# Performance work log

Hardware: AMD Instinct MI355X
Metric: run time of the kernel (lower is better)

## Reference

```python
import jax, jax.numpy as jnp
import numpy as np

KNN = 10       # knn_size
TOPK = 4       # top_k_select
H = 4          # num_heads
HID = 64       # edge-MLP hidden dim


def setup_inputs() -> dict:
    key = jax.random.key(0)
    ks = jax.random.split(key, 12)
    B, V, D = 4, 4096, 256
    s = 0.02
    return {
        "voxel_tokens": jax.random.normal(ks[0], (B, V, D), jnp.float32),
        "voxel_coords": jax.random.uniform(ks[1], (B, V, 3), jnp.float32) * 10.0,
        "mask": jnp.ones((B, V), dtype=bool),
        # EdgeScoringMLP: Linear(2D+3 -> 64), Linear(64 -> 1)
        "W1": jax.random.normal(ks[2], (2 * D + 3, HID), jnp.float32) * s,
        "b1": jnp.zeros((HID,), jnp.float32),
        "W2": jax.random.normal(ks[3], (HID, 1), jnp.float32) * s,
        "b2": jnp.zeros((1,), jnp.float32),
        # CrossAttention projections (D -> D)
        "Wq": jax.random.normal(ks[4], (D, D), jnp.float32) * s,
        "bq": jnp.zeros((D,), jnp.float32),
        "Wk": jax.random.normal(ks[5], (D, D), jnp.float32) * s,
        "bk": jnp.zeros((D,), jnp.float32),
        "Wv": jax.random.normal(ks[6], (D, D), jnp.float32) * s,
        "bv": jnp.zeros((D,), jnp.float32),
        "Wo": jax.random.normal(ks[7], (D, D), jnp.float32) * s,
        "bo": jnp.zeros((D,), jnp.float32),
    }


def reference(voxel_tokens, voxel_coords, mask,
              W1, b1, W2, b2, Wq, bq, Wk, bk, Wv, bv, Wo, bo):
    # mask is all-True (Vp == V per batch element), so the original per-batch
    # loop over dynamic voxel counts is an exact vmap over B. Dropouts are in
    # eval mode (identity).
    D = voxel_tokens.shape[-1]
    Dh = D // H

    def single(tok, coo):  # tok: (V, D), coo: (V, 3)
        # --- KNN graph build (squared euclidean; monotonic in true cdist) ---
        sq = jnp.sum(coo * coo, axis=-1)                        # (V,)
        d2 = sq[:, None] + sq[None, :] - 2.0 * (coo @ coo.T)    # (V, V)
        _, knn = jax.lax.top_k(-d2, KNN + 1)                    # smallest dists
        knn = knn[:, 1:]                                        # drop self, (V, KNN)

        # --- edge features: [anchor_tok, neighbor_tok, rel_pos] ---
        nb_tok = tok[knn]                                       # (V, KNN, D)
        rel = coo[knn] - coo[:, None, :]                        # (V, KNN, 3)
        anchor = jnp.broadcast_to(tok[:, None, :], nb_tok.shape)
        ef = jnp.concatenate([anchor, nb_tok, rel], axis=-1)    # (V, KNN, 2D+3)

        # --- edge-MLP scoring + softmax + top-k edge select ---
        sc = (jax.nn.relu(ef @ W1 + b1) @ W2 + b2)[..., 0]      # (V, KNN)
        aw = jax.nn.softmax(sc, axis=-1)
        _, loc = jax.lax.top_k(aw, TOPK)                        # (V, TOPK)
        sel = jnp.take_along_axis(knn, loc, axis=-1)            # (V, TOPK)
        nbr = tok[sel]                                          # (V, TOPK, D)

        # --- cross attention over selected neighbors ---
        Q = (tok @ Wq + bq).reshape(-1, H, Dh)                  # (V, H, Dh)
        K = (nbr @ Wk + bk).reshape(-1, TOPK, H, Dh)            # (V, TOPK, H, Dh)
        Vv = (nbr @ Wv + bv).reshape(-1, TOPK, H, Dh)
        att = jnp.einsum('vhd,vshd->vhs', Q, K) / jnp.sqrt(jnp.float32(Dh))
        w = jax.nn.softmax(att, axis=-1)                        # (V, H, TOPK)
        out = jnp.einsum('vhs,vshd->vhd', w, Vv).reshape(-1, D)
        return out @ Wo + bo                                    # (V, D)

    return jax.vmap(single)(voxel_tokens, voxel_coords)        # (B, V, D)
```

## Files before the change

### kernel.cpp

```cpp
#include <hip/hip_runtime.h>
#include <hip/hip_bf16.h>

#define VV 4096
#define DDIM 256
#define KNN_K 10
#define TK 4

__device__ __forceinline__ float f_sq3(float x, float y, float z) {
    return __fadd_rn(__fadd_rn(__fmul_rn(x, x), __fmul_rn(y, y)), __fmul_rn(z, z));
}
__device__ __forceinline__ float f_dot3(float ax, float ay, float az,
                                        float bx, float by, float bz) {
    float d = __fmul_rn(ax, bx);
    d = __fmaf_rn(ay, by, d);
    d = __fmaf_rn(az, bz, d);
    return d;
}

__device__ __forceinline__ unsigned long long mkkey(float d2, int j) {
    unsigned u = __float_as_uint(d2);
    u ^= (unsigned)((int)u >> 31) | 0x80000000u;
    return ((unsigned long long)u << 32) | (unsigned)j;
}

__device__ __forceinline__ void fma44(const float4 a, const float4 b, float (&c)[4][4]) {
    c[0][0] = fmaf(a.x, b.x, c[0][0]); c[0][1] = fmaf(a.x, b.y, c[0][1]);
    c[0][2] = fmaf(a.x, b.z, c[0][2]); c[0][3] = fmaf(a.x, b.w, c[0][3]);
    c[1][0] = fmaf(a.y, b.x, c[1][0]); c[1][1] = fmaf(a.y, b.y, c[1][1]);
    c[1][2] = fmaf(a.y, b.z, c[1][2]); c[1][3] = fmaf(a.y, b.w, c[1][3]);
    c[2][0] = fmaf(a.z, b.x, c[2][0]); c[2][1] = fmaf(a.z, b.y, c[2][1]);
    c[2][2] = fmaf(a.z, b.z, c[2][2]); c[2][3] = fmaf(a.z, b.w, c[2][3]);
    c[3][0] = fmaf(a.w, b.x, c[3][0]); c[3][1] = fmaf(a.w, b.y, c[3][1]);
    c[3][2] = fmaf(a.w, b.z, c[3][2]); c[3][3] = fmaf(a.w, b.w, c[3][3]);
}

__global__ void __launch_bounds__(256) qkv_an_gemm_kernel(
    const float* __restrict__ tok,
    const float* __restrict__ Wq, const float* __restrict__ bq,
    const float* __restrict__ Wk, const float* __restrict__ bk,
    const float* __restrict__ Wv, const float* __restrict__ bv,
    const float* __restrict__ W1,
    const float* __restrict__ coords,
    float* __restrict__ qkv,
    float* __restrict__ AN,
    float4* __restrict__ cxyzs)
{
    __shared__ float As[16][68];
    __shared__ float Bs[16][68];

    const int mBlock = blockIdx.x * 64;
    const int by     = blockIdx.y;
    const int tid    = threadIdx.x;
    const bool isAN  = (by >= 12);
    const int  half  = by - 12;

    if (by == 13 && tid < 64) {
        int m = mBlock + tid;
        float x = coords[m * 3 + 0], y = coords[m * 3 + 1], z = coords[m * 3 + 2];
        cxyzs[m] = make_float4(x, y, z, f_sq3(x, y, z));
    }

    const int nBlock = isAN ? 0 : by * 64;
    const int grp    = isAN ? 0 : (nBlock >> 8);
    const int nIn    = nBlock & 255;
    const float* W    = isAN ? (W1 + (size_t)half * 256 * 64)
                             : ((grp == 0) ? Wq : (grp == 1) ? Wk : Wv);
    const float* bias = (grp == 0) ? bq : (grp == 1) ? bk : bv;

    const int tx = tid & 15;
    const int ty = tid >> 4;

    const int ar  = tid >> 2;
    const int ac4 = tid & 3;
    const int br  = tid >> 4;
    const int bc4 = tid & 15;

    float acc[4][4] = {};

    for (int k0 = 0; k0 < 256; k0 += 16) {
        float4 a4 = *(const float4*)&tok[(size_t)(mBlock + ar) * 256 + k0 + ac4 * 4];
        As[ac4 * 4 + 0][ar] = a4.x;
        As[ac4 * 4 + 1][ar] = a4.y;
        As[ac4 * 4 + 2][ar] = a4.z;
        As[ac4 * 4 + 3][ar] = a4.w;
        float4 b4;
        if (isAN) b4 = *(const float4*)&W[(size_t)(k0 + br) * 64 + bc4 * 4];
        else      b4 = *(const float4*)&W[(size_t)(k0 + br) * 256 + nIn + bc4 * 4];
        *(float4*)&Bs[br][bc4 * 4] = b4;
        __syncthreads();
        #pragma unroll
        for (int kk = 0; kk < 16; kk++) {
            float4 av = *(const float4*)&As[kk][ty * 4];
            float4 bv4 = *(const float4*)&Bs[kk][tx * 4];
            fma44(av, bv4, acc);
        }
        __syncthreads();
    }

    if (!isAN) {
        #pragma unroll
        for (int i = 0; i < 4; i++) {
            int m = mBlock + ty * 4 + i;
            float4 o;
            o.x = acc[i][0] + bias[nIn + tx * 4 + 0];
            o.y = acc[i][1] + bias[nIn + tx * 4 + 1];
            o.z = acc[i][2] + bias[nIn + tx * 4 + 2];
            o.w = acc[i][3] + bias[nIn + tx * 4 + 3];
            *(float4*)&qkv[(size_t)m * 768 + nBlock + tx * 4] = o;
        }
    } else {
        #pragma unroll
        for (int i = 0; i < 4; i++) {
            int m = mBlock + ty * 4 + i;
            float4 o;
            o.x = acc[i][0]; o.y = acc[i][1]; o.z = acc[i][2]; o.w = acc[i][3];
            *(float4*)&AN[(size_t)m * 128 + half * 64 + tx * 4] = o;
        }
    }
}

__global__ void __launch_bounds__(256) knn_score_kernel(
    const float* __restrict__ AN,
    const float4* __restrict__ cxyzs,
    const float* __restrict__ W1,
    const float* __restrict__ b1,
    const float* __restrict__ W2,
    int* __restrict__ sel)
{
    const int tid  = threadIdx.x;
    const int lane = tid & 63;
    const int wave = tid >> 6;
    const int q    = blockIdx.x * 4 + wave;
    const int base = q & ~4095;
    const int v    = q & 4095;
    const float4* cx = cxyzs + base;

    __shared__ int   sKnn[4][KNN_K];
    __shared__ float sSc[4][KNN_K];
    __shared__ float sHid[4][KNN_K][65];

    float4 cq = cx[v];
    const float qx = cq.x, qy = cq.y, qz = cq.z, sqq = cq.w;

    unsigned long long best   = ~0ull;
    unsigned long long second = ~0ull;
    unsigned long long used   = 0ull;

    #pragma unroll 4
    for (int i = 0; i < 64; i++) {
        int j = i * 64 + lane;
        float4 c = cx[j];
        float dt  = f_dot3(qx, qy, qz, c.x, c.y, c.z);
        float d2v = __fsub_rn(__fadd_rn(sqq, c.w), __fmul_rn(2.0f, dt));
        unsigned long long k = mkkey(d2v, j);
        if (k < best) { second = best; best = k; }
        else if (k < second) { second = k; }
    }

    #pragma unroll 1
    for (int it = 0; it < 11; it++) {
        unsigned long long rb = best;
        #pragma unroll
        for (int off = 1; off < 64; off <<= 1) {
            unsigned olo = __shfl_xor((unsigned)rb, off);
            unsigned ohi = __shfl_xor((unsigned)(rb >> 32), off);
            unsigned long long o = ((unsigned long long)ohi << 32) | olo;
            if (o < rb) rb = o;
        }
        int wj = (int)((unsigned)rb & 4095u);
        if (it >= 1 && lane == 0) sKnn[wave][it - 1] = wj;

        if ((unsigned)best == (unsigned)rb) {
            used |= 1ull << (wj >> 6);
            best = second;
            second = ~0ull;
            if (best == ~0ull) {
                #pragma unroll 1
                for (int i = 0; i < 64; i++) {
                    if ((used >> i) & 1ull) continue;
                    int j = i * 64 + lane;
                    float4 c = cx[j];
                    float dt  = f_dot3(qx, qy, qz, c.x, c.y, c.z);
                    float d2v = __fsub_rn(__fadd_rn(sqq, c.w), __fmul_rn(2.0f, dt));
                    unsigned long long k = mkkey(d2v, j);
                    if (k < best) { second = best; best = k; }
                    else if (k < second) { second = k; }
                }
            }
        }
    }

    const float sAl = AN[(size_t)q * 128 + lane];
    const float b1l = b1[lane];
    const float wr0 = W1[(512 + 0) * 64 + lane];
    const float wr1 = W1[(512 + 1) * 64 + lane];
    const float wr2 = W1[(512 + 2) * 64 + lane];

    #pragma unroll 1
    for (int nb = 0; nb < KNN_K; nb++) {
        int kn = sKnn[wave][nb];
        float4 cn = cx[kn];
        float acc = __fadd_rn(sAl, AN[(size_t)(base + kn) * 128 + 64 + lane]);
        float rel0 = __fsub_rn(cn.x, qx);
        acc = __fmaf_rn(rel0, wr0, acc);
        float rel1 = __fsub_rn(cn.y, qy);
        acc = __fmaf_rn(rel1, wr1, acc);
        float rel2 = __fsub_rn(cn.z, qz);
        acc = __fmaf_rn(rel2, wr2, acc);
        float hid = __fadd_rn(acc, b1l);
        sHid[wave][nb][lane] = hid > 0.0f ? hid : 0.0f;
    }

    if (lane < KNN_K) {
        float s = 0.0f;
        #pragma unroll 8
        for (int h = 0; h < 64; h++)
            s = __fmaf_rn(sHid[wave][lane][h], W2[h], s);
        sSc[wave][lane] = s;
    }

    if (lane == 0) {
        unsigned um = 0;
        #pragma unroll
        for (int s = 0; s < TK; s++) {
            float bests = -3.4e38f; int bj = 0;
            for (int jj = 0; jj < KNN_K; jj++) {
                if (um & (1u << jj)) continue;
                float sc = sSc[wave][jj];
                if (sc > bests) { bests = sc; bj = jj; }
            }
            um |= 1u << bj;
            sel[(size_t)q * TK + s] = base + sKnn[wave][bj];
        }
    }
}

__global__ void __launch_bounds__(256) attn_gather_kernel(
    const float* __restrict__ qkv, const int* __restrict__ sel,
    float* __restrict__ attnout)
{
    const int q = blockIdx.x;
    const int tid = threadIdx.x;

    const float qv = qkv[(size_t)q * 768 + tid];

    int rows[TK];
    #pragma unroll
    for (int s = 0; s < TK; s++) rows[s] = sel[(size_t)q * TK + s];

    float att[TK];
    #pragma unroll
    for (int s = 0; s < TK; s++) {
        float p = qv * qkv[(size_t)rows[s] * 768 + 256 + tid];
        #pragma unroll
        for (int m = 1; m < 64; m <<= 1) p += __shfl_xor(p, m);
        att[s] = p * 0.125f;
    }

    float mx  = fmaxf(fmaxf(att[0], att[1]), fmaxf(att[2], att[3]));
    float e0 = expf(att[0] - mx), e1 = expf(att[1] - mx),
          e2 = expf(att[2] - mx), e3 = expf(att[3] - mx);
    float inv = 1.0f / (e0 + e1 + e2 + e3);

    float o = (e0 * qkv[(size_t)rows[0] * 768 + 512 + tid] +
               e1 * qkv[(size_t)rows[1] * 768 + 512 + tid] +
               e2 * qkv[(size_t)rows[2] * 768 + 512 + tid] +
               e3 * qkv[(size_t)rows[3] * 768 + 512 + tid]) * inv;

    attnout[(size_t)q * 256 + tid] = o;
}

__global__ void __launch_bounds__(256) wo_gemm_kernel(
    const float* __restrict__ A,
    const float* __restrict__ Wo, const float* __restrict__ bo,
    float* __restrict__ out)
{
    __shared__ float As[16][68];
    __shared__ float Bs[16][68];

    const int mBlock = blockIdx.x * 64;
    const int nBlock = blockIdx.y * 64;

    const int tid = threadIdx.x;
    const int tx = tid & 15;
    const int ty = tid >> 4;

    const int ar  = tid >> 2;
    const int ac4 = tid & 3;
    const int br  = tid >> 4;
    const int bc4 = tid & 15;

    float acc[4][4] = {};

    for (int k0 = 0; k0 < 256; k0 += 16) {
        float4 a4 = *(const float4*)&A[(size_t)(mBlock + ar) * 256 + k0 + ac4 * 4];
        As[ac4 * 4 + 0][ar] = a4.x;
        As[ac4 * 4 + 1][ar] = a4.y;
        As[ac4 * 4 + 2][ar] = a4.z;
        As[ac4 * 4 + 3][ar] = a4.w;
        float4 b4 = *(const float4*)&Wo[(size_t)(k0 + br) * 256 + nBlock + bc4 * 4];
        *(float4*)&Bs[br][bc4 * 4] = b4;
        __syncthreads();
        #pragma unroll
        for (int kk = 0; kk < 16; kk++) {
            float4 av = *(const float4*)&As[kk][ty * 4];
            float4 bv4 = *(const float4*)&Bs[kk][tx * 4];
            fma44(av, bv4, acc);
        }
        __syncthreads();
    }

    #pragma unroll
    for (int i = 0; i < 4; i++) {
        int m = mBlock + ty * 4 + i;
        float4 o;
        o.x = acc[i][0] + bo[nBlock + tx * 4 + 0];
        o.y = acc[i][1] + bo[nBlock + tx * 4 + 1];
        o.z = acc[i][2] + bo[nBlock + tx * 4 + 2];
        o.w = acc[i][3] + bo[nBlock + tx * 4 + 3];
        *(float4*)&out[(size_t)m * 256 + nBlock + tx * 4] = o;
    }
}

__global__ void __launch_bounds__(256) fused_voxel_attn(
    const float* __restrict__ tok,
    const float* __restrict__ coords,
    const float* __restrict__ W1,
    const float* __restrict__ b1,
    const float* __restrict__ W2,
    const float* __restrict__ Wq, const float* __restrict__ bq,
    const float* __restrict__ Wk, const float* __restrict__ bk,
    const float* __restrict__ Wv, const float* __restrict__ bv,
    const float* __restrict__ Wo, const float* __restrict__ bo,
    float* __restrict__ out, int out_size)
{
    const int q    = blockIdx.x;
    const int b    = q >> 12;
    const int v    = q & 4095;
    const int base = q & ~4095;
    const int tid  = threadIdx.x;
    const float* cb = coords + (size_t)b * VV * 3;

    __shared__ float  sval[256];
    __shared__ int    sidx[256];
    __shared__ int    sKnn[KNN_K];
    __shared__ int    sSel[TK];
    __shared__ float  sTokA[DDIM];
    __shared__ float  sTokN[KNN_K][DDIM];
    __shared__ float  sAH[64];
    __shared__ float  sHid[KNN_K][64];
    __shared__ float  sSc[KNN_K];
    __shared__ float  sP[TK][256];
    __shared__ float  sAtt[4][TK];
    __shared__ float  sO[DDIM];

    const float qx = cb[v * 3 + 0];
    const float qy = cb[v * 3 + 1];
    const float qz = cb[v * 3 + 2];
    const float sqq = f_sq3(qx, qy, qz);

    float d2[16];
    #pragma unroll
    for (int i = 0; i < 16; i++) {
        int j = tid + i * 256;
        float xj = cb[j * 3 + 0], yj = cb[j * 3 + 1], zj = cb[j * 3 + 2];
        float sqj = f_sq3(xj, yj, zj);
        float dt  = f_dot3(qx, qy, qz, xj, yj, zj);
        d2[i] = __fsub_rn(__fadd_rn(sqq, sqj), __fmul_rn(2.0f, dt));
    }

    unsigned used = 0;
    for (int it = 0; it < 11; it++) {
        float best = 3.4e38f;
        int bi = 0x7fffffff;
        #pragma unroll
        for (int i = 0; i < 16; i++) {
            if (used & (1u << i)) continue;
            if (d2[i] < best) { best = d2[i]; bi = tid + i * 256; }
        }
        sval[tid] = best;
        sidx[tid] = bi;
        __syncthreads();
        for (int s = 128; s > 0; s >>= 1) {
            if (tid < s) {
                float v2 = sval[tid + s];
                int   i2 = sidx[tid + s];
                if (v2 < sval[tid] || (v2 == sval[tid] && i2 < sidx[tid])) {
                    sval[tid] = v2; sidx[tid] = i2;
                }
            }
            __syncthreads();
        }
        int w = sidx[0] & 4095;
        __syncthreads();
        if (it >= 1 && tid == 0) sKnn[it - 1] = w;
        if ((w & 255) == tid) used |= 1u << (w >> 8);
    }
    __syncthreads();

    sTokA[tid] = tok[(size_t)q * DDIM + tid];
    for (int nb = 0; nb < KNN_K; nb++)
        sTokN[nb][tid] = tok[(size_t)(base + sKnn[nb]) * DDIM + tid];
    __syncthreads();

    if (tid < 64) {
        float a = 0.0f;
        for (int k = 0; k < 256; k++)
            a = __fmaf_rn(sTokA[k], W1[k * 64 + tid], a);
        sAH[tid] = a;
    }
    __syncthreads();

    for (int idx = tid; idx < KNN_K * 64; idx += 256) {
        int nb = idx >> 6;
        int h  = idx & 63;
        float acc = sAH[h];
        const float* tn = sTokN[nb];
        for (int k = 0; k < 256; k++)
            acc = __fmaf_rn(tn[k], W1[(256 + k) * 64 + h], acc);
        #pragma unroll
        for (int c = 0; c < 3; c++) {
            float rel = __fsub_rn(cb[sKnn[nb] * 3 + c], cb[v * 3 + c]);
            acc = __fmaf_rn(rel, W1[(512 + c) * 64 + h], acc);
        }
        float hid = __fadd_rn(acc, b1[h]);
        sHid[nb][h] = hid > 0.0f ? hid : 0.0f;
    }
    __syncthreads();

    if (tid < KNN_K) {
        float s = 0.0f;
        for (int h = 0; h < 64; h++)
            s = __fmaf_rn(sHid[tid][h], W2[h], s);
        sSc[tid] = s;
    }
    __syncthreads();

    if (tid == 0) {
        unsigned um = 0;
        #pragma unroll
        for (int s = 0; s < TK; s++) {
            float best = -3.4e38f; int bj = 0;
            for (int jj = 0; jj < KNN_K; jj++) {
                if (um & (1u << jj)) continue;
                if (sSc[jj] > best) { best = sSc[jj]; bj = jj; }
            }
            um |= 1u << bj;
            sSel[s] = bj;
        }
    }
    __syncthreads();

    int ss[TK];
    float k_acc[TK], v_acc[TK];
    #pragma unroll
    for (int s = 0; s < TK; s++) {
        ss[s] = sSel[s];
        k_acc[s] = bk[tid];
        v_acc[s] = bv[tid];
    }
    float q_acc = bq[tid];

    for (int k = 0; k < 256; k++) {
        float wq = Wq[k * 256 + tid];
        float wk = Wk[k * 256 + tid];
        float wv = Wv[k * 256 + tid];
        q_acc += sTokA[k] * wq;
        #pragma unroll
        for (int s = 0; s < TK; s++) {
            float x = sTokN[ss[s]][k];
            k_acc[s] += x * wk;
            v_acc[s] += x * wv;
        }
    }

    #pragma unroll
    for (int s = 0; s < TK; s++) sP[s][tid] = q_acc * k_acc[s];
    __syncthreads();

    if (tid < 16) {
        int h = tid >> 2, s = tid & 3;
        float p = 0.0f;
        for (int d = 0; d < 64; d++) p += sP[s][h * 64 + d];
        sAtt[h][s] = p * 0.125f;
    }
    __syncthreads();

    const int hh = tid >> 6;
    float a0 = sAtt[hh][0], a1 = sAtt[hh][1], a2 = sAtt[hh][2], a3 = sAtt[hh][3];
    float mx  = fmaxf(fmaxf(a0, a1), fmaxf(a2, a3));
    float e0 = expf(a0 - mx), e1 = expf(a1 - mx), e2 = expf(a2 - mx), e3 = expf(a3 - mx);
    float inv = 1.0f / (e0 + e1 + e2 + e3);
    float o = (e0 * v_acc[0] + e1 * v_acc[1] + e2 * v_acc[2] + e3 * v_acc[3]) * inv;

    sO[tid] = o;
    __syncthreads();

    float a = bo[tid];
    for (int e = 0; e < 256; e++) a += sO[e] * Wo[e * 256 + tid];
    int oidx = q * DDIM + tid;
    if (oidx < out_size)
        out[oidx] = a;
}

extern "C" void kernel_launch(void* const* d_in, const int* in_sizes, int n_in,
                              void* d_out, int out_size, void* d_ws, size_t ws_size,
                              hipStream_t stream)
{
    const long long want[13] = {4194304LL, 49152LL, 32960LL, 64LL, 64LL,
                                65536LL, 256LL, 65536LL, 256LL,
                                65536LL, 256LL, 65536LL, 256LL};
    int idx[13];
    const int n = n_in;

    const long long* s64 = (const long long*)(const void*)in_sizes;
    const int*       s32 = in_sizes;

    bool ok = false;

    if (n >= 13 && s64[0] == want[0]) {
        ok = true;
        int walk = 0;
        for (int t = 0; t < 13; t++) {
            int f = -1;
            for (int i = walk; i < n; i++) {
                if (s64[i] == want[t]) { f = i; break; }
            }
            if (f < 0) { ok = false; break; }
            idx[t] = f; walk = f + 1;
        }
    }

    if (!ok) {
        ok = true;
        int walk = 0;
        for (int t = 0; t < 13; t++) {
            int f = -1;
            for (int i = walk; i < n; i++) {
                if ((long long)s32[i] == want[t]) { f = i; break; }
            }
            if (f < 0) { ok = false; break; }
            idx[t] = f; walk = f + 1;
        }
    }

    if (!ok) return;

    const float* tok    = (const float*)d_in[idx[0]];
    const float* coords = (const float*)d_in[idx[1]];
    const float* W1     = (const float*)d_in[idx[2]];
    const float* b1     = (const float*)d_in[idx[3]];
    const float* W2     = (const float*)d_in[idx[4]];
    const float* Wq     = (const float*)d_in[idx[5]];
    const float* bq     = (const float*)d_in[idx[6]];
    const float* Wk     = (const float*)d_in[idx[7]];
    const float* bk     = (const float*)d_in[idx[8]];
    const float* Wv     = (const float*)d_in[idx[9]];
    const float* bv     = (const float*)d_in[idx[10]];
    const float* Wo     = (const float*)d_in[idx[11]];
    const float* bo     = (const float*)d_in[idx[12]];
    float* out = (float*)d_out;

    const size_t NEED = 67633152;
    if (ws_size >= NEED) {
        char* ws = (char*)d_ws;
        int*    sel     = (int*)   (ws + 0);
        float*  AN      = (float*) (ws + 262144);
        float*  attnout = (float*) (ws + 262144);
        float*  qkv     = (float*) (ws + 17039360);
        float4* cxyzs   = (float4*)(ws + 67371008);

        qkv_an_gemm_kernel<<<dim3(256, 14), dim3(256), 0, stream>>>(
            tok, Wq, bq, Wk, bk, Wv, bv, W1, coords, qkv, AN, cxyzs);
        knn_score_kernel<<<dim3(4096), dim3(256), 0, stream>>>(AN, cxyzs, W1, b1, W2, sel);
        attn_gather_kernel<<<dim3(16384), dim3(256), 0, stream>>>(qkv, sel, attnout);
        wo_gemm_kernel<<<dim3(256, 4), dim3(256), 0, stream>>>(attnout, Wo, bo, out);
    } else {
        fused_voxel_attn<<<dim3(16384), dim3(256), 0, stream>>>(
            tok, coords, W1, b1, W2, Wq, bq, Wk, bk, Wv, bv, Wo, bo, out, out_size);
    }
}
```

Baseline: 367.8 us.

## Use uniform grid spatial hashing for KNN search with brute-force fallback

Adds a per-batch grid build kernel that bins voxel coordinates into a 16^3 cell grid with a counting sort. The KNN kernel then scans only the 5x5x5 neighbouring cells around each query instead of all 4096 points, and checks whether the 11th-nearest distance lies inside a conservative bound. If that check fails, or any lane holds more than 64 candidates, it falls back to the original brute-force scan. This targets the O(V^2) distance computation, at the cost of an extra small kernel, irregular per-lane loops, and a grid sized for the coordinate range [0,10).

```diff
diff --git a/kernel.cpp b/kernel.cpp
--- a/kernel.cpp
+++ b/kernel.cpp
@@ -5,6 +5,10 @@
 #define DDIM 256
 #define KNN_K 10
 #define TK 4
+
+#define GCELLS 16
+#define GINV   1.6f
+#define TIER_BNDSQ 1.54f
 
 __device__ __forceinline__ float f_sq3(float x, float y, float z) {
     return __fadd_rn(__fadd_rn(__fmul_rn(x, x), __fmul_rn(y, y)), __fmul_rn(z, z));
@@ -21,6 +25,11 @@
     unsigned u = __float_as_uint(d2);
     u ^= (unsigned)((int)u >> 31) | 0x80000000u;
     return ((unsigned long long)u << 32) | (unsigned)j;
+}
+
+__device__ __forceinline__ int cell1(float x) {
+    int c = (int)(x * GINV);
+    return c > 15 ? 15 : (c < 0 ? 0 : c);
 }
 
 __device__ __forceinline__ void fma44(const float4 a, const float4 b, float (&c)[4][4]) {
@@ -32,6 +41,58 @@
     c[2][2] = fmaf(a.z, b.z, c[2][2]); c[2][3] = fmaf(a.z, b.w, c[2][3]);
     c[3][0] = fmaf(a.w, b.x, c[3][0]); c[3][1] = fmaf(a.w, b.y, c[3][1]);
     c[3][2] = fmaf(a.w, b.z, c[3][2]); c[3][3] = fmaf(a.w, b.w, c[3][3]);
+}
+
+__global__ void __launch_bounds__(256) grid_build_kernel(
+    const float* __restrict__ coords,
+    int* __restrict__ cellOff,
+    int* __restrict__ sortedIdx)
+{
+    const int b   = blockIdx.x;
+    const int tid = threadIdx.x;
+    const float* cb = coords + (size_t)b * VV * 3;
+    int* cOff = cellOff + b * 4097;
+    int* sIdx = sortedIdx + b * 4096;
+
+    __shared__ int hist[4096];
+    __shared__ int part[256];
+
+    for (int i = tid; i < 4096; i += 256) hist[i] = 0;
+    __syncthreads();
+
+    for (int p = tid; p < 4096; p += 256) {
+        int c = (cell1(cb[p * 3 + 0]) * 16 + cell1(cb[p * 3 + 1])) * 16 + cell1(cb[p * 3 + 2]);
+        atomicAdd(&hist[c], 1);
+    }
+    __syncthreads();
+
+    int loc[16];
+    int sum = 0;
+    const int bi = tid * 16;
+    #pragma unroll
+    for (int k = 0; k < 16; k++) { loc[k] = hist[bi + k]; sum += loc[k]; }
+    part[tid] = sum;
+    __syncthreads();
+    for (int off = 1; off < 256; off <<= 1) {
+        int vv = (tid >= off) ? part[tid - off] : 0;
+        __syncthreads();
+        part[tid] += vv;
+        __syncthreads();
+    }
+    int run = part[tid] - sum;
+    #pragma unroll
+    for (int k = 0; k < 16; k++) { int t2 = loc[k]; hist[bi + k] = run; run += t2; }
+    __syncthreads();
+
+    for (int i = tid; i < 4096; i += 256) cOff[i] = hist[i];
+    if (tid == 0) cOff[4096] = 4096;
+    __syncthreads();
+
+    for (int p = tid; p < 4096; p += 256) {
+        int c = (cell1(cb[p * 3 + 0]) * 16 + cell1(cb[p * 3 + 1])) * 16 + cell1(cb[p * 3 + 2]);
+        int pos = atomicAdd(&hist[c], 1);
+        sIdx[pos] = p;
+    }
 }
 
 __global__ void __launch_bounds__(256) qkv_an_gemm_kernel(
@@ -69,7 +130,6 @@
 
     const int tx = tid & 15;
     const int ty = tid >> 4;
-
     const int ar  = tid >> 2;
     const int ac4 = tid & 3;
     const int br  = tid >> 4;
@@ -122,6 +182,8 @@
 __global__ void __launch_bounds__(256) knn_score_kernel(
     const float* __restrict__ AN,
     const float4* __restrict__ cxyzs,
+    const int* __restrict__ cellOff,
+    const int* __restrict__ sortedIdx,
     const float* __restrict__ W1,
     const float* __restrict__ b1,
     const float* __restrict__ W2,
@@ -131,9 +193,12 @@
     const int lane = tid & 63;
     const int wave = tid >> 6;
     const int q    = blockIdx.x * 4 + wave;
+    const int b    = q >> 12;
     const int base = q & ~4095;
     const int v    = q & 4095;
     const float4* cx = cxyzs + base;
+    const int* cOff = cellOff + b * 4097;
+    const int* sIdx = sortedIdx + b * 4096;
 
     __shared__ int   sKnn[4][KNN_K];
     __shared__ float sSc[4][KNN_K];
@@ -141,50 +206,140 @@
 
     float4 cq = cx[v];
     const float qx = cq.x, qy = cq.y, qz = cq.z, sqq = cq.w;
-
-    unsigned long long best   = ~0ull;
-    unsigned long long second = ~0ull;
-    unsigned long long used   = 0ull;
-
-    #pragma unroll 4
-    for (int i = 0; i < 64; i++) {
-        int j = i * 64 + lane;
-        float4 c = cx[j];
-        float dt  = f_dot3(qx, qy, qz, c.x, c.y, c.z);
-        float d2v = __fsub_rn(__fadd_rn(sqq, c.w), __fmul_rn(2.0f, dt));
-        unsigned long long k = mkkey(d2v, j);
-        if (k < best) { second = best; best = k; }
-        else if (k < second) { second = k; }
-    }
+    const int qcx = cell1(qx), qcy = cell1(qy), qcz = cell1(qz);
+
+    unsigned long long best = ~0ull, second = ~0ull, used = 0ull;
+    int bOrd = 0x7fffffff, sOrd = 0x7fffffff;
+    int ordEnd = 0;
 
     #pragma unroll 1
-    for (int it = 0; it < 11; it++) {
-        unsigned long long rb = best;
-        #pragma unroll
-        for (int off = 1; off < 64; off <<= 1) {
-            unsigned olo = __shfl_xor((unsigned)rb, off);
-            unsigned ohi = __shfl_xor((unsigned)(rb >> 32), off);
-            unsigned long long o = ((unsigned long long)ohi << 32) | olo;
-            if (o < rb) rb = o;
-        }
-        int wj = (int)((unsigned)rb & 4095u);
-        if (it >= 1 && lane == 0) sKnn[wave][it - 1] = wj;
-
-        if ((unsigned)best == (unsigned)rb) {
-            used |= 1ull << (wj >> 6);
-            best = second;
-            second = ~0ull;
-            if (best == ~0ull) {
+    for (int ci = 0; ci < 2; ci++) {
+        int t = lane + ci * 64;
+        if (t < 125) {
+            int dz = t / 25 - 2;
+            int rem = t - (t / 25) * 25;
+            int dy = rem / 5 - 2;
+            int dx = rem - (rem / 5) * 5 - 2;
+            int cxi = qcx + dx, cyi = qcy + dy, czi = qcz + dz;
+            if ((unsigned)cxi < 16u && (unsigned)cyi < 16u && (unsigned)czi < 16u) {
+                int cell = (cxi * 16 + cyi) * 16 + czi;
+                int s = cOff[cell], e = cOff[cell + 1];
                 #pragma unroll 1
-                for (int i = 0; i < 64; i++) {
-                    if ((used >> i) & 1ull) continue;
-                    int j = i * 64 + lane;
+                for (int p = s; p < e; p++) {
+                    int j = sIdx[p];
                     float4 c = cx[j];
-                    float dt  = f_dot3(qx, qy, qz, c.x, c.y, c.z);
-                    float d2v = __fsub_rn(__fadd_rn(sqq, c.w), __fmul_rn(2.0f, dt));
-                    unsigned long long k = mkkey(d2v, j);
-                    if (k < best) { second = best; best = k; }
-                    else if (k < second) { second = k; }
+                    float dt = f_dot3(qx, qy, qz, c.x, c.y, c.z);
+                    float d  = __fsub_rn(__fadd_rn(sqq, c.w), __fmul_rn(2.0f, dt));
+                    unsigned long long k = mkkey(d, j);
+                    if (k < best)        { second = best; sOrd = bOrd; best = k; bOrd = ordEnd; }
+                    else if (k < second) { second = k; sOrd = ordEnd; }
+                    ordEnd++;
+                }
+            }
+        }
+    }
+
+    bool tierOk = (__ballot(ordEnd > 64) == 0ull);
+
+    unsigned long long key11 = ~0ull;
+    if (tierOk) {
+        #pragma unroll 1
+        for (int it = 0; it < 11; it++) {
+            unsigned long long rb = best;
+            #pragma unroll
+            for (int off = 1; off < 64; off <<= 1) {
+                unsigned olo = __shfl_xor((unsigned)rb, off);
+                unsigned ohi = __shfl_xor((unsigned)(rb >> 32), off);
+                unsigned long long o = ((unsigned long long)ohi << 32) | olo;
+                if (o < rb) rb = o;
+            }
+            int wj = (int)((unsigned)rb & 4095u);
+            if (it >= 1 && lane == 0) sKnn[wave][it - 1] = wj;
+            if (it == 10) key11 = rb;
+
+            if ((unsigned)best == (unsigned)rb && best != ~0ull) {
+                used |= 1ull << bOrd;
+                best = second; bOrd = sOrd;
+                second = ~0ull; sOrd = 0x7fffffff;
+                if (best == ~0ull) {
+                    int ord = 0;
+                    #pragma unroll 1
+                    for (int ci = 0; ci < 2; ci++) {
+                        int t = lane + ci * 64;
+                        if (t < 125) {
+                            int dz = t / 25 - 2;
+                            int rem = t - (t / 25) * 25;
+                            int dy = rem / 5 - 2;
+                            int dx = rem - (rem / 5) * 5 - 2;
+                            int cxi = qcx + dx, cyi = qcy + dy, czi = qcz + dz;
+                            if ((unsigned)cxi < 16u && (unsigned)cyi < 16u && (unsigned)czi < 16u) {
+                                int cell = (cxi * 16 + cyi) * 16 + czi;
+                                int s = cOff[cell], e = cOff[cell + 1];
+                                #pragma unroll 1
+                                for (int p = s; p < e; p++) {
+                                    if (!((used >> ord) & 1ull)) {
+                                        int j = sIdx[p];
+                                        float4 c = cx[j];
+                                        float dt = f_dot3(qx, qy, qz, c.x, c.y, c.z);
+                                        float d  = __fsub_rn(__fadd_rn(sqq, c.w), __fmul_rn(2.0f, dt));
+                                        unsigned long long k = mkkey(d, j);
+                                        if (k < best)        { second = best; sOrd = bOrd; best = k; bOrd = ord; }
+                                        else if (k < second) { second = k; sOrd = ord; }
+                                    }
+                                    ord++;
+                                }
+                            }
+                        }
+                    }
+                }
+            }
+        }
+        unsigned uu = (unsigned)(key11 >> 32);
+        uu = (uu & 0x80000000u) ? (uu ^ 0x80000000u) : ~uu;
+        float d11 = __uint_as_float(uu);
+        tierOk = (key11 != ~0ull) && (d11 < TIER_BNDSQ);
+    }
+
+    if (!tierOk) {
+        unsigned long long fb = ~0ull, fs = ~0ull, fused = 0ull;
+        #pragma unroll 4
+        for (int i = 0; i < 64; i++) {
+            int j = i * 64 + lane;
+            float4 c = cx[j];
+            float dt  = f_dot3(qx, qy, qz, c.x, c.y, c.z);
+            float d2v = __fsub_rn(__fadd_rn(sqq, c.w), __fmul_rn(2.0f, dt));
+            unsigned long long k = mkkey(d2v, j);
+            if (k < fb) { fs = fb; fb = k; }
+            else if (k < fs) { fs = k; }
+        }
+        #pragma unroll 1
+        for (int it = 0; it < 11; it++) {
+            unsigned long long rb = fb;
+            #pragma unroll
+            for (int off = 1; off < 64; off <<= 1) {
+                unsigned olo = __shfl_xor((unsigned)rb, off);
+                unsigned ohi = __shfl_xor((unsigned)(rb >> 32), off);
+                unsigned long long o = ((unsigned long long)ohi << 32) | olo;
+                if (o < rb) rb = o;
+            }
+            int wj = (int)((unsigned)rb & 4095u);
+            if (it >= 1 && lane == 0) sKnn[wave][it - 1] = wj;
+            if ((unsigned)fb == (unsigned)rb) {
+                fused |= 1ull << (wj >> 6);
+                fb = fs;
+                fs = ~0ull;
+                if (fb == ~0ull) {
+                    #pragma unroll 1
+                    for (int i = 0; i < 64; i++) {
+                        if ((fused >> i) & 1ull) continue;
+                        int j = i * 64 + lane;
+                        float4 c = cx[j];
+                        float dt  = f_dot3(qx, qy, qz, c.x, c.y, c.z);
+                        float d2v = __fsub_rn(__fadd_rn(sqq, c.w), __fmul_rn(2.0f, dt));
+                        unsigned long long k = mkkey(d2v, j);
+                        if (k < fb) { fs = fb; fb = k; }
+                        else if (k < fs) { fs = k; }
+                    }
                 }
             }
         }
@@ -561,7 +716,7 @@
     const float* bo     = (const float*)d_in[idx[12]];
     float* out = (float*)d_out;
 
-    const size_t NEED = 67633152;
+    const size_t NEED = 67764240;
     if (ws_size >= NEED) {
         char* ws = (char*)d_ws;
         int*    sel     = (int*)   (ws + 0);
@@ -569,10 +724,14 @@
         float*  attnout = (float*) (ws + 262144);
         float*  qkv     = (float*) (ws + 17039360);
         float4* cxyzs   = (float4*)(ws + 67371008);
-
+        int*    cellOff = (int*)   (ws + 67633152);
+        int*    sortIdx = (int*)   (ws + 67698704);
+
+        grid_build_kernel<<<dim3(4), dim3(256), 0, stream>>>(coords, cellOff, sortIdx);
         qkv_an_gemm_kernel<<<dim3(256, 14), dim3(256), 0, stream>>>(
             tok, Wq, bq, Wk, bk, Wv, bv, W1, coords, qkv, AN, cxyzs);
-        knn_score_kernel<<<dim3(4096), dim3(256), 0, stream>>>(AN, cxyzs, W1, b1, W2, sel);
+        knn_score_kernel<<<dim3(4096), dim3(256), 0, stream>>>(
+            AN, cxyzs, cellOff, sortIdx, W1, b1, W2, sel);
         attn_gather_kernel<<<dim3(16384), dim3(256), 0, stream>>>(qkv, sel, attnout);
         wo_gemm_kernel<<<dim3(256, 4), dim3(256), 0, stream>>>(attnout, Wo, bo, out);
     } else {
```

Result: faster. 346.1 us (-5.9%).
